# Kernel tuning notes

Hardware: AMD Instinct MI355X
Metric: run time of the kernel (lower is better)

Reference implementation:

```python
import jax, jax.numpy as jnp
import numpy as np

B, Q, H = 1, 1024, 2048
NH, NKV, HD = 32, 8, 64
KB = 2048
THETA = 10000.0
KB_MAX_TRAIN = 4096.0


def _bitlinear(x, w):
    """BitNet b1.58 linear: per-token int8 absmax activation quant + ternary weight quant (STE)."""
    a_scale = 127.0 / jnp.clip(jnp.max(jnp.abs(x), axis=-1, keepdims=True), 1e-5)
    xq = jnp.clip(jnp.round(x * a_scale), -128.0, 127.0) / a_scale
    w_scale = 1.0 / jnp.clip(jnp.mean(jnp.abs(w)), 1e-5)
    wq = jnp.clip(jnp.round(w * w_scale), -1.0, 1.0) / w_scale
    x_ste = x + jax.lax.stop_gradient(xq - x)
    w_ste = w + jax.lax.stop_gradient(wq - w)
    return jnp.einsum('bsh,oh->bso', x_ste, w_ste)


def _rope_cos_sin(position_ids):
    inv_freq = 1.0 / (THETA ** (jnp.arange(0, HD, 2, dtype=jnp.float32) / HD))  # [HD/2]
    freqs = position_ids.astype(jnp.float32)[..., None] * inv_freq  # [B,Q,HD/2]
    emb = jnp.concatenate([freqs, freqs], axis=-1)  # [B,Q,HD]
    return jnp.cos(emb)[:, None], jnp.sin(emb)[:, None]  # [B,1,Q,HD]


def _rotate_half(x):
    return jnp.concatenate([-x[..., HD // 2:], x[..., :HD // 2]], axis=-1)


def setup_inputs() -> dict:
    key = jax.random.key(0)
    ks = jax.random.split(key, 9)
    hidden_states = jax.random.normal(ks[0], (B, Q, H), jnp.float32)
    # additive causal mask
    attention_mask = jnp.triu(jnp.full((Q, Q), -1e9, jnp.float32), 1)[None, None]
    kb_keys = jax.random.normal(ks[1], (B, NH, KB, HD), jnp.float32)
    kb_values = jax.random.normal(ks[2], (B, NH, KB, HD), jnp.float32)
    s = 0.02
    Wq = jax.random.normal(ks[3], (NH * HD, H), jnp.float32) * s
    Wk = jax.random.normal(ks[4], (NKV * HD, H), jnp.float32) * s
    Wv = jax.random.normal(ks[5], (NKV * HD, H), jnp.float32) * s
    Wo = jax.random.normal(ks[6], (H, NH * HD), jnp.float32) * s
    Wq_new = jax.random.normal(ks[7], (NH * HD, H), jnp.float32) * s
    position_ids = jnp.arange(Q, dtype=jnp.int32)[None, :]
    return dict(hidden_states=hidden_states, attention_mask=attention_mask,
                kb_keys=kb_keys, kb_values=kb_values,
                Wq=Wq, Wk=Wk, Wv=Wv, Wo=Wo, Wq_new=Wq_new,
                position_ids=position_ids)


def reference(hidden_states, attention_mask, kb_keys, kb_values,
              Wq, Wk, Wv, Wo, Wq_new, position_ids):
    b, q_len, _ = hidden_states.shape
    # BitLinear QKV projections
    q = _bitlinear(hidden_states, Wq).reshape(b, q_len, NH, HD).transpose(0, 2, 1, 3)
    k = _bitlinear(hidden_states, Wk).reshape(b, q_len, NKV, HD).transpose(0, 2, 1, 3)
    v = _bitlinear(hidden_states, Wv).reshape(b, q_len, NKV, HD).transpose(0, 2, 1, 3)
    # RoPE on prompt q/k (KB query is NOT rotated, matching the source)
    cos, sin = _rope_cos_sin(position_ids)
    q = q * cos + _rotate_half(q) * sin
    k = k * cos + _rotate_half(k) * sin
    # GQA: repeat kv heads
    groups = NH // NKV
    k = jnp.repeat(k, groups, axis=1)
    v = jnp.repeat(v, groups, axis=1)
    # KB query via separate BitLinear
    kb_q = _bitlinear(hidden_states, Wq_new).reshape(b, q_len, NH, HD).transpose(0, 2, 1, 3)
    scale = 1.0 / jnp.sqrt(jnp.float32(HD))
    kb_len = kb_keys.shape[2]
    scores_kb = jnp.einsum('bhqd,bhkd->bhqk', kb_q, kb_keys) * scale
    scores_kb = scores_kb + (jnp.log(jnp.float32(KB_MAX_TRAIN)) - jnp.log(jnp.float32(kb_len)))
    scores_p = jnp.einsum('bhqd,bhkd->bhqk', q, k) * scale + attention_mask
    attn = jax.nn.softmax(jnp.concatenate([scores_kb, scores_p], axis=-1).astype(jnp.float32), axis=-1)
    out = (jnp.einsum('bhqk,bhkd->bhqd', attn[..., :kb_len], kb_values)
           + jnp.einsum('bhqk,bhkd->bhqd', attn[..., kb_len:], v))
    out = out.transpose(0, 2, 1, 3).reshape(b, q_len, NH * HD)
    return _bitlinear(out, Wo)
```

## Files before the change

kernel.cpp:

```cpp
#include <hip/hip_runtime.h>
#include <hip/hip_bf16.h>
#include <stdint.h>
#include <math.h>

#define cH    2048
#define cQ    1024
#define cNH   32
#define cNKV  8
#define cKB   2048

#define INV_BIG   (1.0f/4194304.0f)
#define INV_SMALL (1.0f/1048576.0f)

#define WS_SUMS 0
#define WS_DQ1  256
#define WS_DQ2  4352
#define WS_XQ   8448
#define WS_WALL 4202752
#define WS_QB   25174272
#define WS_KB   33562880
#define WS_VB   35660032
#define WS_QN   37757184
#define WS_ROPET 46145792

using short8  = __attribute__((ext_vector_type(8))) short;
using floatx4 = __attribute__((ext_vector_type(4))) float;

__device__ __forceinline__ void bsplit(float x, unsigned short& hi, unsigned short& lo) {
  __hip_bfloat16 h = __float2bfloat16(x);
  float hf = __bfloat162float(h);
  __hip_bfloat16 l = __float2bfloat16(x - hf);
  hi = *(unsigned short*)&h;
  lo = *(unsigned short*)&l;
}

__device__ __forceinline__ unsigned short tern(float v, float ws) {
  float q = rintf(v * ws);
  q = fminf(fmaxf(q, -1.0f), 1.0f);
  return (unsigned short)(__float_as_uint(q) >> 16);
}

__device__ __forceinline__ void gload16(const void* g, void* l) {
  __builtin_amdgcn_global_load_lds((const __attribute__((address_space(1))) void*)g,
                                   (__attribute__((address_space(3))) void*)l, 16, 0, 0);
}

__global__ void k_ropetab(const int* __restrict__ pos, float2* __restrict__ tab) {
  int i = blockIdx.x * 256 + threadIdx.x;
  int t = i >> 5, d = i & 31;
  double p = (double)pos[t];
  double ang = p * pow(10000.0, -(double)d / 32.0);
  tab[i] = make_float2((float)cos(ang), (float)sin(ang));
}

__global__ void k_abssum5(const float* __restrict__ w0, const float* __restrict__ w1,
                          const float* __restrict__ w2, const float* __restrict__ w3,
                          const float* __restrict__ w4, double* __restrict__ out) {
  __shared__ double red[256];
  const int seg = blockIdx.y;
  const float* w = seg == 0 ? w0 : seg == 1 ? w1 : seg == 2 ? w2 : seg == 3 ? w3 : w4;
  const int n4 = ((seg == 1 || seg == 2) ? 512 * 2048 : 2048 * 2048) / 4;
  double s = 0.0;
  for (int i = blockIdx.x * 256 + threadIdx.x; i < n4; i += gridDim.x * 256) {
    float4 x = *(const float4*)(w + (size_t)i * 4);
    s += (double)fabsf(x.x) + (double)fabsf(x.y) + (double)fabsf(x.z) + (double)fabsf(x.w);
  }
  red[threadIdx.x] = s;
  __syncthreads();
  for (int o = 128; o > 0; o >>= 1) {
    if ((int)threadIdx.x < o) red[threadIdx.x] += red[threadIdx.x + o];
    __syncthreads();
  }
  if (threadIdx.x == 0) atomicAdd(out + seg, red[0]);
}

__global__ void k_wquant4(const float* __restrict__ Wq, const float* __restrict__ Wk,
                          const float* __restrict__ Wv, const float* __restrict__ Wqn,
                          unsigned short* __restrict__ wall, const double* __restrict__ sums) {
  size_t i = ((size_t)blockIdx.x * 256 + threadIdx.x) * 4;
  const float* src; size_t off; double s; float inv;
  if (i < 4194304)      { src = Wq;  off = 0;       s = sums[0]; inv = INV_BIG; }
  else if (i < 5242880) { src = Wk;  off = 4194304; s = sums[1]; inv = INV_SMALL; }
  else if (i < 6291456) { src = Wv;  off = 5242880; s = sums[2]; inv = INV_SMALL; }
  else                  { src = Wqn; off = 6291456; s = sums[4]; inv = INV_BIG; }
  float ws = 1.0f / fmaxf((float)s * inv, 1e-5f);
  float4 x = *(const float4*)(src + (i - off));
  ushort4 o;
  o.x = tern(x.x, ws); o.y = tern(x.y, ws); o.z = tern(x.z, ws); o.w = tern(x.w, ws);
  *(ushort4*)(wall + i) = o;
}

__global__ void k_wquant(const float* __restrict__ w, unsigned short* __restrict__ wq,
                         const double* __restrict__ sum, float inv_n) {
  size_t i = ((size_t)blockIdx.x * 256 + threadIdx.x) * 4;
  float ws = 1.0f / fmaxf((float)(*sum) * inv_n, 1e-5f);
  float4 x = *(const float4*)(w + i);
  ushort4 o;
  o.x = tern(x.x, ws); o.y = tern(x.y, ws); o.z = tern(x.z, ws); o.w = tern(x.w, ws);
  *(ushort4*)(wq + i) = o;
}

__global__ void k_aquant(const float* __restrict__ x, unsigned short* __restrict__ xq,
                         float* __restrict__ dq, int K) {
  int t = blockIdx.x;
  const float4* xr = (const float4*)(x + (size_t)t * K);
  const int K4 = K / 4;
  __shared__ float red[256];
  float m = 0.0f;
  for (int i = threadIdx.x; i < K4; i += 256) {
    float4 v = xr[i];
    m = fmaxf(m, fmaxf(fmaxf(fabsf(v.x), fabsf(v.y)), fmaxf(fabsf(v.z), fabsf(v.w))));
  }
  red[threadIdx.x] = m;
  __syncthreads();
  for (int o = 128; o > 0; o >>= 1) {
    if ((int)threadIdx.x < o) red[threadIdx.x] = fmaxf(red[threadIdx.x], red[threadIdx.x + o]);
    __syncthreads();
  }
  float amax = fmaxf(red[0], 1e-5f);
  float as = 127.0f / amax;
  ushort4* xo = (ushort4*)(xq + (size_t)t * K);
  for (int i = threadIdx.x; i < K4; i += 256) {
    float4 v = xr[i];
    ushort4 o;
    float q;
    q = fminf(fmaxf(rintf(v.x * as), -128.0f), 127.0f); o.x = (unsigned short)(__float_as_uint(q) >> 16);
    q = fminf(fmaxf(rintf(v.y * as), -128.0f), 127.0f); o.y = (unsigned short)(__float_as_uint(q) >> 16);
    q = fminf(fmaxf(rintf(v.z * as), -128.0f), 127.0f); o.z = (unsigned short)(__float_as_uint(q) >> 16);
    q = fminf(fmaxf(rintf(v.w * as), -128.0f), 127.0f); o.w = (unsigned short)(__float_as_uint(q) >> 16);
    xo[i] = o;
  }
  if (threadIdx.x == 0) dq[t] = amax / 127.0f;
}

__global__ __launch_bounds__(256) void k_gemm_mfma(
    const unsigned short* __restrict__ Aq, const unsigned short* __restrict__ Ball,
    const float* __restrict__ adq, const double* __restrict__ sums,
    const float2* __restrict__ ropetab,
    float* __restrict__ oQ, unsigned short* __restrict__ oKhi,
    unsigned short* __restrict__ oKlo,
    float* __restrict__ oV, float* __restrict__ oQN, int mode) {
  __shared__ unsigned short As[128 * 72];
  __shared__ unsigned short Bs[128 * 72];
  const int t = threadIdx.x;
  const int lane = t & 63;
  const int row16 = lane & 15, q = lane >> 4;
  const int w = t >> 6;
  const int wm = (w >> 1) * 64, wn = (w & 1) * 64;
  const int bx = blockIdx.x;
  const int m0 = blockIdx.y * 128;
  const unsigned short* Bp = Ball + (size_t)bx * 128 * 2048;

  floatx4 acc[4][4];
#pragma unroll
  for (int g = 0; g < 4; ++g)
#pragma unroll
    for (int h = 0; h < 4; ++h) acc[g][h] = (floatx4){0.f, 0.f, 0.f, 0.f};

  for (int k0 = 0; k0 < 2048; k0 += 64) {
#pragma unroll
    for (int i = 0; i < 4; ++i) {
      int c = t + 256 * i;
      int row = c >> 3, g8 = c & 7;
      *(uint4*)&As[row * 72 + g8 * 8] =
          *(const uint4*)(Aq + (size_t)(m0 + row) * 2048 + k0 + g8 * 8);
      *(uint4*)&Bs[row * 72 + g8 * 8] =
          *(const uint4*)(Bp + (size_t)row * 2048 + k0 + g8 * 8);
    }
    __syncthreads();
#pragma unroll
    for (int kk = 0; kk < 2; ++kk) {
      short8 af[4], bf[4];
#pragma unroll
      for (int g = 0; g < 4; ++g)
        af[g] = *(const short8*)&As[(wm + g * 16 + row16) * 72 + kk * 32 + q * 8];
#pragma unroll
      for (int h = 0; h < 4; ++h)
        bf[h] = *(const short8*)&Bs[(wn + h * 16 + row16) * 72 + kk * 32 + q * 8];
#pragma unroll
      for (int g = 0; g < 4; ++g)
#pragma unroll
        for (int h = 0; h < 4; ++h)
          acc[g][h] = __builtin_amdgcn_mfma_f32_16x16x32_bf16(af[g], bf[h], acc[g][h], 0, 0, 0);
    }
    __syncthreads();
  }

  float* outp = nullptr; int Nout = 0, nb0; float wdq;
  if (mode == 1)      { outp = oQ;  Nout = 2048; nb0 = bx * 128;        wdq = fmaxf((float)sums[3] * INV_BIG,   1e-5f); }
  else if (bx < 16)   { outp = oQ;  Nout = 2048; nb0 = bx * 128;        wdq = fmaxf((float)sums[0] * INV_BIG,   1e-5f); }
  else if (bx < 20)   {             Nout = 512;  nb0 = (bx - 16) * 128; wdq = fmaxf((float)sums[1] * INV_SMALL, 1e-5f); }
  else if (bx < 24)   { outp = oV;  Nout = 512;  nb0 = (bx - 20) * 128; wdq = fmaxf((float)sums[2] * INV_SMALL, 1e-5f); }
  else                { outp = oQN; Nout = 2048; nb0 = (bx - 24) * 128; wdq = fmaxf((float)sums[4] * INV_BIG,   1e-5f); }

  if (mode == 0 && bx < 20) {
#pragma unroll
    for (int g = 0; g < 4; ++g)
#pragma unroll
      for (int r = 0; r < 4; ++r) {
        int m = m0 + wm + g * 16 + q * 4 + r;
        float s = adq[m] * wdq;
        float2 cs0 = ropetab[m * 32 + row16];
        float2 cs1 = ropetab[m * 32 + 16 + row16];
        float v0 = acc[g][0][r] * s, v1 = acc[g][1][r] * s;
        float v2 = acc[g][2][r] * s, v3 = acc[g][3][r] * s;
        float o0 = v0 * cs0.x - v2 * cs0.y;
        float o2 = v2 * cs0.x + v0 * cs0.y;
        float o1 = v1 * cs1.x - v3 * cs1.y;
        float o3 = v3 * cs1.x + v1 * cs1.y;
        if (bx < 16) {
          size_t base = (size_t)m * Nout + nb0 + wn;
          outp[base + row16]      = o0;
          outp[base + 16 + row16] = o1;
          outp[base + 32 + row16] = o2;
          outp[base + 48 + row16] = o3;
        } else {
          int hkv_ = (nb0 + wn) >> 6;
          int kt_ = m >> 6, rr = m & 63, sb = rr & 7;
          size_t tb = ((size_t)(hkv_ * 16 + kt_)) * 4096 + (size_t)rr * 64;
          int s0 = row16 >> 3, j0 = row16 & 7;
          unsigned short hi, lo; int ix;
          bsplit(o0, hi, lo); ix = (((0 + s0) ^ sb) << 3) + j0; oKhi[tb + ix] = hi; oKlo[tb + ix] = lo;
          bsplit(o1, hi, lo); ix = (((2 + s0) ^ sb) << 3) + j0; oKhi[tb + ix] = hi; oKlo[tb + ix] = lo;
          bsplit(o2, hi, lo); ix = (((4 + s0) ^ sb) << 3) + j0; oKhi[tb + ix] = hi; oKlo[tb + ix] = lo;
          bsplit(o3, hi, lo); ix = (((6 + s0) ^ sb) << 3) + j0; oKhi[tb + ix] = hi; oKlo[tb + ix] = lo;
        }
      }
  } else {
#pragma unroll
    for (int g = 0; g < 4; ++g)
#pragma unroll
      for (int r = 0; r < 4; ++r) {
        int m = m0 + wm + g * 16 + q * 4 + r;
        float s = adq[m] * wdq;
#pragma unroll
        for (int h = 0; h < 4; ++h)
          outp[(size_t)m * Nout + nb0 + wn + h * 16 + row16] = acc[g][h][r] * s;
      }
  }
}

__global__ __launch_bounds__(256) void k_prep(
    const float* __restrict__ kbv, const float* __restrict__ Vb,
    unsigned short* __restrict__ vtKBhi, unsigned short* __restrict__ vtPhi,
    float* __restrict__ kbk) {
  const int b = blockIdx.x;
  const int t = threadIdx.x;
  if (b >= 1152) {
    float* tile = kbk + (size_t)(b - 1152) * 4096;
    float v[2][8];
#pragma unroll
    for (int u = 0; u < 2; ++u) {
      int task = t + 256 * u;
      int r = task >> 3, s = task & 7;
      *(float4*)&v[u][0] = *(const float4*)(tile + r * 64 + s * 8);
      *(float4*)&v[u][4] = *(const float4*)(tile + r * 64 + s * 8 + 4);
    }
    __syncthreads();
    unsigned short* up = (unsigned short*)tile;
#pragma unroll
    for (int u = 0; u < 2; ++u) {
      int task = t + 256 * u;
      int r = task >> 3, s = task & 7;
      union { unsigned short u16[8]; uint4 q; } hi, lo;
#pragma unroll
      for (int j = 0; j < 8; ++j) bsplit(v[u][j], hi.u16[j], lo.u16[j]);
      size_t off = (size_t)r * 64 + ((s ^ (r & 7)) << 3);
      *(uint4*)(up + off)        = hi.q;
      *(uint4*)(up + 4096 + off) = lo.q;
    }
    return;
  }
  __shared__ float Lf[64 * 65];
  const float* src; unsigned short *dhi, *dlo; int srcStride;
  if (b < 1024) {
    int h = b >> 5, kt = b & 31;
    src = kbv + ((size_t)h * cKB + kt * 64) * 64; srcStride = 64;
    dhi = vtKBhi + (size_t)b * 4096; dlo = dhi + 4194304;
  } else {
    int bb = b - 1024;
    int hkv = bb >> 4, kt = bb & 15;
    src = Vb + (size_t)(kt * 64) * 512 + hkv * 64; srcStride = 512;
    dhi = vtPhi + (size_t)bb * 4096; dlo = dhi + 524288;
  }
#pragma unroll
  for (int i = 0; i < 4; ++i) {
    int c = t + 256 * i;
    int row = c >> 4, c4 = (c & 15) * 4;
    float4 x = *(const float4*)(src + (size_t)row * srcStride + c4);
    Lf[row * 65 + c4 + 0] = x.x;
    Lf[row * 65 + c4 + 1] = x.y;
    Lf[row * 65 + c4 + 2] = x.z;
    Lf[row * 65 + c4 + 3] = x.w;
  }
  __syncthreads();
#pragma unroll
  for (int u = 0; u < 2; ++u) {
    int task = t + 256 * u;
    int d = task >> 3, s = task & 7;
    union { unsigned short u16[8]; uint4 q; } hi, lo;
#pragma unroll
    for (int j = 0; j < 8; ++j) bsplit(Lf[(s * 8 + j) * 65 + d], hi.u16[j], lo.u16[j]);
    size_t off = (size_t)d * 64 + ((s ^ (d & 7)) << 3);
    *(uint4*)(dhi + off) = hi.q;
    *(uint4*)(dlo + off) = lo.q;
  }
}

__global__ __launch_bounds__(256, 3) void k_attn_mfma(
    const float* __restrict__ Qr, float* qnctx,
    const unsigned short* __restrict__ KPhi,
    const unsigned short* __restrict__ kbkS,
    const unsigned short* __restrict__ vtKBhi,
    const unsigned short* __restrict__ vtPhi) {
  __shared__ __attribute__((aligned(16))) unsigned short Khi[4096], Klo[4096];
  __shared__ __attribute__((aligned(16))) unsigned short Vhi[4096], Vlo[4096];
  __shared__ __attribute__((aligned(16))) unsigned int Pbuf[4][16 * 68];

  const int t = threadIdx.x;
  const int lane = t & 63;
  const int col = lane & 15;
  const int quad = lane >> 4;
  const int w = t >> 6;
  const int h = blockIdx.x;
  const int q0 = blockIdx.y * 64;
  const int hkv = h >> 2;
  const float kbbias = 0.69314718055994531f;
  unsigned int* Pw = &Pbuf[w][0];
  const int cb = col * 64;
  const int sw0 = ((quad    ) ^ (col & 7)) << 3;
  const int sw1 = ((quad + 4) ^ (col & 7)) << 3;
  const int so = w * 1024 + lane * 8;

  short8 qh[2], ql[2];
  auto load_q = [&](const float* base) {
#pragma unroll
    for (int kk = 0; kk < 2; ++kk) {
      const float* p = base + (size_t)(q0 + w * 16 + col) * 2048 + h * 64 + kk * 32 + quad * 8;
      float4 a = *(const float4*)p;
      float4 b = *(const float4*)(p + 4);
      float xs[8] = {a.x, a.y, a.z, a.w, b.x, b.y, b.z, b.w};
#pragma unroll
      for (int j = 0; j < 8; ++j) {
        unsigned short hi, lo;
        bsplit(xs[j] * 0.125f, hi, lo);
        qh[kk][j] = (short)hi;
        ql[kk][j] = (short)lo;
      }
    }
  };
  load_q(qnctx);

  floatx4 acco[4];
  float m_[4], l_[4];
#pragma unroll
  for (int nt = 0; nt < 4; ++nt) acco[nt] = (floatx4){0.f, 0.f, 0.f, 0.f};
#pragma unroll
  for (int r = 0; r < 4; ++r) { m_[r] = -3.0e38f; l_[r] = 0.f; }

  const int ntiles = 32 + (q0 >> 6) + 1;
  for (int kt = 0; kt < ntiles; ++kt) {
    const bool isKB = kt < 32;
    const int k0 = isKB ? kt * 64 : (kt - 32) * 64;
    if (kt == 32) load_q(Qr);

    {
      const unsigned short *sKhi, *sKlo, *sVhi, *sVlo;
      if (isKB) {
        const size_t tk = (size_t)(h * 32 + kt);
        sKhi = kbkS + tk * 8192;   sKlo = sKhi + 4096;
        sVhi = vtKBhi + tk * 4096; sVlo = sVhi + 4194304;
      } else {
        const size_t tk = (size_t)(hkv * 16 + (kt - 32));
        sKhi = KPhi + tk * 4096;   sKlo = sKhi + 524288;
        sVhi = vtPhi + tk * 4096;  sVlo = sVhi + 524288;
      }
      gload16(sKhi + so,       &Khi[w * 1024]);
      gload16(sKhi + so + 512, &Khi[w * 1024 + 512]);
      gload16(sKlo + so,       &Klo[w * 1024]);
      gload16(sKlo + so + 512, &Klo[w * 1024 + 512]);
      gload16(sVhi + so,       &Vhi[w * 1024]);
      gload16(sVhi + so + 512, &Vhi[w * 1024 + 512]);
      gload16(sVlo + so,       &Vlo[w * 1024]);
      gload16(sVlo + so + 512, &Vlo[w * 1024 + 512]);
    }
    __syncthreads();

    floatx4 accs[4];
#pragma unroll
    for (int nt = 0; nt < 4; ++nt) accs[nt] = (floatx4){0.f, 0.f, 0.f, 0.f};
#pragma unroll
    for (int kk = 0; kk < 2; ++kk) {
      const int swk = kk ? sw1 : sw0;
#pragma unroll
      for (int nt = 0; nt < 4; ++nt) {
        const int ko = nt * 1024 + cb + swk;
        short8 khh = *(const short8*)&Khi[ko];
        short8 kll = *(const short8*)&Klo[ko];
        accs[nt] = __builtin_amdgcn_mfma_f32_16x16x32_bf16(qh[kk], khh, accs[nt], 0, 0, 0);
        accs[nt] = __builtin_amdgcn_mfma_f32_16x16x32_bf16(ql[kk], khh, accs[nt], 0, 0, 0);
        accs[nt] = __builtin_amdgcn_mfma_f32_16x16x32_bf16(qh[kk], kll, accs[nt], 0, 0, 0);
      }
    }

    float sv[4][4];
#pragma unroll
    for (int nt = 0; nt < 4; ++nt) {
      int kg = k0 + nt * 16 + col;
#pragma unroll
      for (int r = 0; r < 4; ++r) {
        int qg = q0 + w * 16 + quad * 4 + r;
        float b = isKB ? kbbias : ((kg <= qg) ? 0.0f : -1e9f);
        sv[nt][r] = accs[nt][r] + b;
      }
    }
#pragma unroll
    for (int r = 0; r < 4; ++r) {
      float rmax = fmaxf(fmaxf(sv[0][r], sv[1][r]), fmaxf(sv[2][r], sv[3][r]));
#pragma unroll
      for (int off = 8; off; off >>= 1) rmax = fmaxf(rmax, __shfl_xor(rmax, off));
      float mnew = fmaxf(m_[r], rmax);
      float alpha = __expf(m_[r] - mnew);
      float psum = 0.f;
#pragma unroll
      for (int nt = 0; nt < 4; ++nt) {
        float p = __expf(sv[nt][r] - mnew);
        sv[nt][r] = p;
        psum += p;
      }
#pragma unroll
      for (int off = 8; off; off >>= 1) psum += __shfl_xor(psum, off);
      l_[r] = l_[r] * alpha + psum;
      m_[r] = mnew;
#pragma unroll
      for (int nt = 0; nt < 4; ++nt) acco[nt][r] *= alpha;
    }

#pragma unroll
    for (int nt = 0; nt < 4; ++nt)
#pragma unroll
      for (int r = 0; r < 4; ++r) {
        unsigned xb = __float_as_uint(sv[nt][r]);
        float hf = __uint_as_float(xb & 0xffff0000u);
        unsigned db = __float_as_uint(sv[nt][r] - hf);
        Pw[(quad * 4 + r) * 68 + nt * 16 + col] = (xb >> 16) | (db & 0xffff0000u);
      }

#pragma unroll
    for (int kk = 0; kk < 2; ++kk) {
      uint4 pa = *(const uint4*)&Pw[col * 68 + kk * 32 + quad * 8];
      uint4 pb = *(const uint4*)&Pw[col * 68 + kk * 32 + quad * 8 + 4];
      union { unsigned int u[4]; short8 s; } uh, ul;
      uh.u[0] = (pa.x & 0xffffu) | (pa.y << 16);
      uh.u[1] = (pa.z & 0xffffu) | (pa.w << 16);
      uh.u[2] = (pb.x & 0xffffu) | (pb.y << 16);
      uh.u[3] = (pb.z & 0xffffu) | (pb.w << 16);
      ul.u[0] = (pa.x >> 16) | (pa.y & 0xffff0000u);
      ul.u[1] = (pa.z >> 16) | (pa.w & 0xffff0000u);
      ul.u[2] = (pb.x >> 16) | (pb.y & 0xffff0000u);
      ul.u[3] = (pb.z >> 16) | (pb.w & 0xffff0000u);
      short8 ph8 = uh.s, pl8 = ul.s;
      const int swk = kk ? sw1 : sw0;
#pragma unroll
      for (int nt = 0; nt < 4; ++nt) {
        const int vo = nt * 1024 + cb + swk;
        short8 vhh = *(const short8*)&Vhi[vo];
        short8 vll = *(const short8*)&Vlo[vo];
        acco[nt] = __builtin_amdgcn_mfma_f32_16x16x32_bf16(ph8, vhh, acco[nt], 0, 0, 0);
        acco[nt] = __builtin_amdgcn_mfma_f32_16x16x32_bf16(pl8, vhh, acco[nt], 0, 0, 0);
        acco[nt] = __builtin_amdgcn_mfma_f32_16x16x32_bf16(ph8, vll, acco[nt], 0, 0, 0);
      }
    }
    __syncthreads();
  }

#pragma unroll
  for (int r = 0; r < 4; ++r) {
    float linv = 1.0f / l_[r];
#pragma unroll
    for (int nt = 0; nt < 4; ++nt)
      qnctx[(size_t)(q0 + w * 16 + quad * 4 + r) * 2048 + h * 64 + nt * 16 + col] =
          acco[nt][r] * linv;
  }
}

extern "C" void kernel_launch(void* const* d_in, const int* in_sizes, int n_in,
                              void* d_out, int out_size, void* d_ws, size_t ws_size,
                              hipStream_t stream) {
  (void)in_sizes; (void)n_in; (void)out_size; (void)ws_size;
  const float* hidden = (const float*)d_in[0];
  float* kbk = (float*)d_in[2];
  const float* kbv = (const float*)d_in[3];
  const float* Wq  = (const float*)d_in[4];
  const float* Wk  = (const float*)d_in[5];
  const float* Wv  = (const float*)d_in[6];
  const float* Wo  = (const float*)d_in[7];
  const float* Wqn = (const float*)d_in[8];
  const int*   pos = (const int*)d_in[9];

  char* ws = (char*)d_ws;
  double* sums = (double*)(ws + WS_SUMS);
  float* dq1 = (float*)(ws + WS_DQ1);
  float* dq2 = (float*)(ws + WS_DQ2);
  unsigned short* xq   = (unsigned short*)(ws + WS_XQ);
  unsigned short* wall = (unsigned short*)(ws + WS_WALL);
  unsigned short* vtKBhi = (unsigned short*)(ws + WS_WALL);
  unsigned short* vtPhi  = (unsigned short*)(ws + WS_WALL + 16777216);
  unsigned short* wqo  = (unsigned short*)(ws + WS_QB);
  float* Qb  = (float*)(ws + WS_QB);
  unsigned short* KPhi = (unsigned short*)(ws + WS_KB);
  unsigned short* KPlo = KPhi + 524288;
  float* Vb  = (float*)(ws + WS_VB);
  float* QNC = (float*)(ws + WS_QN);
  float2* ropetab = (float2*)(ws + WS_ROPET);

  hipMemsetAsync(sums, 0, 64, stream);

  k_ropetab<<<128, 256, 0, stream>>>(pos, ropetab);
  k_abssum5<<<dim3(128, 5), 256, 0, stream>>>(Wq, Wk, Wv, Wo, Wqn, sums);
  k_wquant4<<<10240, 256, 0, stream>>>(Wq, Wk, Wv, Wqn, wall, sums);
  k_aquant<<<cQ, 256, 0, stream>>>(hidden, xq, dq1, cH);

  k_gemm_mfma<<<dim3(40, 8), 256, 0, stream>>>(xq, wall, dq1, sums, ropetab,
                                               Qb, KPhi, KPlo, Vb, QNC, 0);

  k_prep<<<1152 + 1024, 256, 0, stream>>>(kbv, Vb, vtKBhi, vtPhi, kbk);

  k_attn_mfma<<<dim3(cNH, cQ / 64), 256, 0, stream>>>(
      Qb, QNC, KPhi, (const unsigned short*)kbk, vtKBhi, vtPhi);

  k_wquant<<<4096, 256, 0, stream>>>(Wo, wqo, sums + 3, INV_BIG);
  k_aquant<<<cQ, 256, 0, stream>>>(QNC, xq, dq2, cH);

  k_gemm_mfma<<<dim3(16, 8), 256, 0, stream>>>(xq, wqo, dq2, sums, ropetab,
                                               (float*)d_out, nullptr, nullptr,
                                               nullptr, nullptr, 1);
}
```

Baseline: 396.7 us.

## Double-buffer K/V tiles in attention kernel with async prefetch and priority hints

Doubles the LDS K/V buffers so the next tile's global-to-LDS loads are issued before computing on the current tile, replacing __syncthreads with explicit vmcnt waits and barriers. Both Q variants are loaded up front, mask arithmetic is specialized so only the diagonal tile applies causal masking, the P buffer uses an XOR swizzle instead of padding, and s_setprio wraps the MFMA blocks. The larger LDS footprint lowers launch bounds from 3 to 2 blocks per CU, trading occupancy for overlap. The extra Q registers add register pressure.

```diff
diff --git a/kernel.cpp b/kernel.cpp
--- a/kernel.cpp
+++ b/kernel.cpp
@@ -307,15 +307,15 @@
   }
 }
 
-__global__ __launch_bounds__(256, 3) void k_attn_mfma(
+__global__ __launch_bounds__(256, 2) void k_attn_mfma(
     const float* __restrict__ Qr, float* qnctx,
     const unsigned short* __restrict__ KPhi,
     const unsigned short* __restrict__ kbkS,
     const unsigned short* __restrict__ vtKBhi,
     const unsigned short* __restrict__ vtPhi) {
-  __shared__ __attribute__((aligned(16))) unsigned short Khi[4096], Klo[4096];
-  __shared__ __attribute__((aligned(16))) unsigned short Vhi[4096], Vlo[4096];
-  __shared__ __attribute__((aligned(16))) unsigned int Pbuf[4][16 * 68];
+  __shared__ __attribute__((aligned(16))) unsigned short Khi[2][4096], Klo[2][4096];
+  __shared__ __attribute__((aligned(16))) unsigned short Vhi[2][4096], Vlo[2][4096];
+  __shared__ __attribute__((aligned(16))) unsigned int Pbuf[4][16 * 64];
 
   const int t = threadIdx.x;
   const int lane = t & 63;
@@ -332,24 +332,59 @@
   const int sw1 = ((quad + 4) ^ (col & 7)) << 3;
   const int so = w * 1024 + lane * 8;
 
-  short8 qh[2], ql[2];
-  auto load_q = [&](const float* base) {
+  const int prow = quad * 4;
+  const int pf_r = col & 7;
+  const int prd0 = col * 64;
+
+  short8 qAh[2], qAl[2];
+  short8 qBh[2], qBl[2];
+  {
+    const float* baseA = qnctx;
+    const float* baseB = Qr;
 #pragma unroll
     for (int kk = 0; kk < 2; ++kk) {
-      const float* p = base + (size_t)(q0 + w * 16 + col) * 2048 + h * 64 + kk * 32 + quad * 8;
-      float4 a = *(const float4*)p;
-      float4 b = *(const float4*)(p + 4);
+      const size_t off = (size_t)(q0 + w * 16 + col) * 2048 + h * 64 + kk * 32 + quad * 8;
+      float4 a = *(const float4*)(baseA + off);
+      float4 b = *(const float4*)(baseA + off + 4);
       float xs[8] = {a.x, a.y, a.z, a.w, b.x, b.y, b.z, b.w};
 #pragma unroll
       for (int j = 0; j < 8; ++j) {
         unsigned short hi, lo;
         bsplit(xs[j] * 0.125f, hi, lo);
-        qh[kk][j] = (short)hi;
-        ql[kk][j] = (short)lo;
-      }
-    }
+        qAh[kk][j] = (short)hi; qAl[kk][j] = (short)lo;
+      }
+      float4 c = *(const float4*)(baseB + off);
+      float4 d = *(const float4*)(baseB + off + 4);
+      float ys[8] = {c.x, c.y, c.z, c.w, d.x, d.y, d.z, d.w};
+#pragma unroll
+      for (int j = 0; j < 8; ++j) {
+        unsigned short hi, lo;
+        bsplit(ys[j] * 0.125f, hi, lo);
+        qBh[kk][j] = (short)hi; qBl[kk][j] = (short)lo;
+      }
+    }
+  }
+
+  auto stage = [&](int kt2, int bsel) {
+    const unsigned short *sKhi, *sKlo, *sVhi, *sVlo;
+    if (kt2 < 32) {
+      const size_t tk = (size_t)(h * 32 + kt2);
+      sKhi = kbkS + tk * 8192;   sKlo = sKhi + 4096;
+      sVhi = vtKBhi + tk * 4096; sVlo = sVhi + 4194304;
+    } else {
+      const size_t tk = (size_t)(hkv * 16 + (kt2 - 32));
+      sKhi = KPhi + tk * 4096;   sKlo = sKhi + 524288;
+      sVhi = vtPhi + tk * 4096;  sVlo = sVhi + 524288;
+    }
+    gload16(sKhi + so,       &Khi[bsel][w * 1024]);
+    gload16(sKhi + so + 512, &Khi[bsel][w * 1024 + 512]);
+    gload16(sKlo + so,       &Klo[bsel][w * 1024]);
+    gload16(sKlo + so + 512, &Klo[bsel][w * 1024 + 512]);
+    gload16(sVhi + so,       &Vhi[bsel][w * 1024]);
+    gload16(sVhi + so + 512, &Vhi[bsel][w * 1024 + 512]);
+    gload16(sVlo + so,       &Vlo[bsel][w * 1024]);
+    gload16(sVlo + so + 512, &Vlo[bsel][w * 1024 + 512]);
   };
-  load_q(qnctx);
 
   floatx4 acco[4];
   float m_[4], l_[4];
@@ -359,59 +394,73 @@
   for (int r = 0; r < 4; ++r) { m_[r] = -3.0e38f; l_[r] = 0.f; }
 
   const int ntiles = 32 + (q0 >> 6) + 1;
+  stage(0, 0);
+
   for (int kt = 0; kt < ntiles; ++kt) {
+    const int cur = kt & 1;
     const bool isKB = kt < 32;
     const int k0 = isKB ? kt * 64 : (kt - 32) * 64;
-    if (kt == 32) load_q(Qr);
-
-    {
-      const unsigned short *sKhi, *sKlo, *sVhi, *sVlo;
-      if (isKB) {
-        const size_t tk = (size_t)(h * 32 + kt);
-        sKhi = kbkS + tk * 8192;   sKlo = sKhi + 4096;
-        sVhi = vtKBhi + tk * 4096; sVlo = sVhi + 4194304;
-      } else {
-        const size_t tk = (size_t)(hkv * 16 + (kt - 32));
-        sKhi = KPhi + tk * 4096;   sKlo = sKhi + 524288;
-        sVhi = vtPhi + tk * 4096;  sVlo = sVhi + 524288;
-      }
-      gload16(sKhi + so,       &Khi[w * 1024]);
-      gload16(sKhi + so + 512, &Khi[w * 1024 + 512]);
-      gload16(sKlo + so,       &Klo[w * 1024]);
-      gload16(sKlo + so + 512, &Klo[w * 1024 + 512]);
-      gload16(sVhi + so,       &Vhi[w * 1024]);
-      gload16(sVhi + so + 512, &Vhi[w * 1024 + 512]);
-      gload16(sVlo + so,       &Vlo[w * 1024]);
-      gload16(sVlo + so + 512, &Vlo[w * 1024 + 512]);
-    }
-    __syncthreads();
+    const int pfkt = (kt + 1 < ntiles) ? kt + 1 : kt;
+    stage(pfkt, cur ^ 1);
+    asm volatile("s_waitcnt vmcnt(8)" ::: "memory");
+    __builtin_amdgcn_s_barrier();
+    asm volatile("" ::: "memory");
 
     floatx4 accs[4];
 #pragma unroll
     for (int nt = 0; nt < 4; ++nt) accs[nt] = (floatx4){0.f, 0.f, 0.f, 0.f};
-#pragma unroll
-    for (int kk = 0; kk < 2; ++kk) {
-      const int swk = kk ? sw1 : sw0;
+    __builtin_amdgcn_s_setprio(1);
+    if (isKB) {
+#pragma unroll
+      for (int kk = 0; kk < 2; ++kk) {
+        const int swk = kk ? sw1 : sw0;
+#pragma unroll
+        for (int nt = 0; nt < 4; ++nt) {
+          const int ko = nt * 1024 + cb + swk;
+          short8 khh = *(const short8*)&Khi[cur][ko];
+          short8 kll = *(const short8*)&Klo[cur][ko];
+          accs[nt] = __builtin_amdgcn_mfma_f32_16x16x32_bf16(qAh[kk], khh, accs[nt], 0, 0, 0);
+          accs[nt] = __builtin_amdgcn_mfma_f32_16x16x32_bf16(qAl[kk], khh, accs[nt], 0, 0, 0);
+          accs[nt] = __builtin_amdgcn_mfma_f32_16x16x32_bf16(qAh[kk], kll, accs[nt], 0, 0, 0);
+        }
+      }
+    } else {
+#pragma unroll
+      for (int kk = 0; kk < 2; ++kk) {
+        const int swk = kk ? sw1 : sw0;
+#pragma unroll
+        for (int nt = 0; nt < 4; ++nt) {
+          const int ko = nt * 1024 + cb + swk;
+          short8 khh = *(const short8*)&Khi[cur][ko];
+          short8 kll = *(const short8*)&Klo[cur][ko];
+          accs[nt] = __builtin_amdgcn_mfma_f32_16x16x32_bf16(qBh[kk], khh, accs[nt], 0, 0, 0);
+          accs[nt] = __builtin_amdgcn_mfma_f32_16x16x32_bf16(qBl[kk], khh, accs[nt], 0, 0, 0);
+          accs[nt] = __builtin_amdgcn_mfma_f32_16x16x32_bf16(qBh[kk], kll, accs[nt], 0, 0, 0);
+        }
+      }
+    }
+    __builtin_amdgcn_s_setprio(0);
+
+    float sv[4][4];
+    if (isKB) {
+#pragma unroll
+      for (int nt = 0; nt < 4; ++nt)
+#pragma unroll
+        for (int r = 0; r < 4; ++r) sv[nt][r] = accs[nt][r] + kbbias;
+    } else if (kt < ntiles - 1) {
+#pragma unroll
+      for (int nt = 0; nt < 4; ++nt)
+#pragma unroll
+        for (int r = 0; r < 4; ++r) sv[nt][r] = accs[nt][r];
+    } else {
 #pragma unroll
       for (int nt = 0; nt < 4; ++nt) {
-        const int ko = nt * 1024 + cb + swk;
-        short8 khh = *(const short8*)&Khi[ko];
-        short8 kll = *(const short8*)&Klo[ko];
-        accs[nt] = __builtin_amdgcn_mfma_f32_16x16x32_bf16(qh[kk], khh, accs[nt], 0, 0, 0);
-        accs[nt] = __builtin_amdgcn_mfma_f32_16x16x32_bf16(ql[kk], khh, accs[nt], 0, 0, 0);
-        accs[nt] = __builtin_amdgcn_mfma_f32_16x16x32_bf16(qh[kk], kll, accs[nt], 0, 0, 0);
-      }
-    }
-
-    float sv[4][4];
-#pragma unroll
-    for (int nt = 0; nt < 4; ++nt) {
-      int kg = k0 + nt * 16 + col;
-#pragma unroll
-      for (int r = 0; r < 4; ++r) {
-        int qg = q0 + w * 16 + quad * 4 + r;
-        float b = isKB ? kbbias : ((kg <= qg) ? 0.0f : -1e9f);
-        sv[nt][r] = accs[nt][r] + b;
+        int kl = nt * 16 + col;
+#pragma unroll
+        for (int r = 0; r < 4; ++r) {
+          int ql = w * 16 + quad * 4 + r;
+          sv[nt][r] = accs[nt][r] + ((kl <= ql) ? 0.0f : -1e9f);
+        }
       }
     }
 #pragma unroll
@@ -443,13 +492,17 @@
         unsigned xb = __float_as_uint(sv[nt][r]);
         float hf = __uint_as_float(xb & 0xffff0000u);
         unsigned db = __float_as_uint(sv[nt][r] - hf);
-        Pw[(quad * 4 + r) * 68 + nt * 16 + col] = (xb >> 16) | (db & 0xffff0000u);
+        int row = prow + r;
+        int cu = nt * 16 + col;
+        int slot = cu >> 2, j = cu & 3;
+        Pw[row * 64 + ((((slot ^ (row & 7)) << 2)) | j)] = (xb >> 16) | (db & 0xffff0000u);
       }
 
 #pragma unroll
     for (int kk = 0; kk < 2; ++kk) {
-      uint4 pa = *(const uint4*)&Pw[col * 68 + kk * 32 + quad * 8];
-      uint4 pb = *(const uint4*)&Pw[col * 68 + kk * 32 + quad * 8 + 4];
+      const int s0 = kk * 8 + quad * 2;
+      uint4 pa = *(const uint4*)&Pw[prd0 + (((s0) ^ pf_r) << 2)];
+      uint4 pb = *(const uint4*)&Pw[prd0 + (((s0 + 1) ^ pf_r) << 2)];
       union { unsigned int u[4]; short8 s; } uh, ul;
       uh.u[0] = (pa.x & 0xffffu) | (pa.y << 16);
       uh.u[1] = (pa.z & 0xffffu) | (pa.w << 16);
@@ -461,18 +514,23 @@
       ul.u[3] = (pb.z >> 16) | (pb.w & 0xffff0000u);
       short8 ph8 = uh.s, pl8 = ul.s;
       const int swk = kk ? sw1 : sw0;
+      __builtin_amdgcn_s_setprio(1);
 #pragma unroll
       for (int nt = 0; nt < 4; ++nt) {
         const int vo = nt * 1024 + cb + swk;
-        short8 vhh = *(const short8*)&Vhi[vo];
-        short8 vll = *(const short8*)&Vlo[vo];
+        short8 vhh = *(const short8*)&Vhi[cur][vo];
+        short8 vll = *(const short8*)&Vlo[cur][vo];
         acco[nt] = __builtin_amdgcn_mfma_f32_16x16x32_bf16(ph8, vhh, acco[nt], 0, 0, 0);
         acco[nt] = __builtin_amdgcn_mfma_f32_16x16x32_bf16(pl8, vhh, acco[nt], 0, 0, 0);
         acco[nt] = __builtin_amdgcn_mfma_f32_16x16x32_bf16(ph8, vll, acco[nt], 0, 0, 0);
       }
-    }
-    __syncthreads();
-  }
+      __builtin_amdgcn_s_setprio(0);
+    }
+    asm volatile("s_waitcnt lgkmcnt(0)" ::: "memory");
+    __builtin_amdgcn_s_barrier();
+    asm volatile("" ::: "memory");
+  }
+  asm volatile("s_waitcnt vmcnt(0)" ::: "memory");
 
 #pragma unroll
   for (int r = 0; r < 4; ++r) {
```

After: 405.3 us. 2.2% more time.

## Load K/V fragments directly into registers in MFMA-fragment layout, prefetch next K

Applied to the files above, without the earlier changes.

The prep and projection kernels now write K and V^T tiles in a layout that matches the per-lane MFMA operand order. The attention kernel then loads K/V fragments straight from global memory into registers instead of staging them through LDS. This removes the LDS staging buffers and most block barriers. The next K tile is prefetched during the softmax/PV phase, both query variants are kept in registers, and the causal mask is applied only on the diagonal tile. The cost is higher register pressure, so launch bounds drop occupancy from 3 to 2 blocks per CU, and each wave issues its own global loads with no LDS sharing.

```diff
diff --git a/kernel.cpp b/kernel.cpp
--- a/kernel.cpp
+++ b/kernel.cpp
@@ -23,6 +23,7 @@
 #define WS_QN   37757184
 #define WS_ROPET 46145792
 
+
 using short8  = __attribute__((ext_vector_type(8))) short;
 using floatx4 = __attribute__((ext_vector_type(4))) float;
 
@@ -38,11 +39,6 @@
   float q = rintf(v * ws);
   q = fminf(fmaxf(q, -1.0f), 1.0f);
   return (unsigned short)(__float_as_uint(q) >> 16);
-}
-
-__device__ __forceinline__ void gload16(const void* g, void* l) {
-  __builtin_amdgcn_global_load_lds((const __attribute__((address_space(1))) void*)g,
-                                   (__attribute__((address_space(3))) void*)l, 16, 0, 0);
 }
 
 __global__ void k_ropetab(const int* __restrict__ pos, float2* __restrict__ tab) {
@@ -216,14 +212,15 @@
           outp[base + 48 + row16] = o3;
         } else {
           int hkv_ = (nb0 + wn) >> 6;
-          int kt_ = m >> 6, rr = m & 63, sb = rr & 7;
-          size_t tb = ((size_t)(hkv_ * 16 + kt_)) * 4096 + (size_t)rr * 64;
-          int s0 = row16 >> 3, j0 = row16 & 7;
+          int kt_ = m >> 6, rr = m & 63;
+          size_t tb = ((size_t)(hkv_ * 16 + kt_)) * 4096;
+          int lbase = (rr & 15) + ((row16 >> 3) << 4);
+          int ntb = (rr >> 4) * 512 + (row16 & 7);
           unsigned short hi, lo; int ix;
-          bsplit(o0, hi, lo); ix = (((0 + s0) ^ sb) << 3) + j0; oKhi[tb + ix] = hi; oKlo[tb + ix] = lo;
-          bsplit(o1, hi, lo); ix = (((2 + s0) ^ sb) << 3) + j0; oKhi[tb + ix] = hi; oKlo[tb + ix] = lo;
-          bsplit(o2, hi, lo); ix = (((4 + s0) ^ sb) << 3) + j0; oKhi[tb + ix] = hi; oKlo[tb + ix] = lo;
-          bsplit(o3, hi, lo); ix = (((6 + s0) ^ sb) << 3) + j0; oKhi[tb + ix] = hi; oKlo[tb + ix] = lo;
+          bsplit(o0, hi, lo); ix = ntb + (lbase     ) * 8;          oKhi[tb + ix] = hi; oKlo[tb + ix] = lo;
+          bsplit(o1, hi, lo); ix = ntb + (lbase + 32) * 8;          oKhi[tb + ix] = hi; oKlo[tb + ix] = lo;
+          bsplit(o2, hi, lo); ix = ntb + (lbase     ) * 8 + 2048;   oKhi[tb + ix] = hi; oKlo[tb + ix] = lo;
+          bsplit(o3, hi, lo); ix = ntb + (lbase + 32) * 8 + 2048;   oKhi[tb + ix] = hi; oKlo[tb + ix] = lo;
         }
       }
   } else {
@@ -265,7 +262,7 @@
       union { unsigned short u16[8]; uint4 q; } hi, lo;
 #pragma unroll
       for (int j = 0; j < 8; ++j) bsplit(v[u][j], hi.u16[j], lo.u16[j]);
-      size_t off = (size_t)r * 64 + ((s ^ (r & 7)) << 3);
+      size_t off = (size_t)(((s >> 2) * 4 + (r >> 4)) * 512 + ((r & 15) + ((s & 3) << 4)) * 8);
       *(uint4*)(up + off)        = hi.q;
       *(uint4*)(up + 4096 + off) = lo.q;
     }
@@ -301,20 +298,18 @@
     union { unsigned short u16[8]; uint4 q; } hi, lo;
 #pragma unroll
     for (int j = 0; j < 8; ++j) bsplit(Lf[(s * 8 + j) * 65 + d], hi.u16[j], lo.u16[j]);
-    size_t off = (size_t)d * 64 + ((s ^ (d & 7)) << 3);
+    size_t off = (size_t)(((s >> 2) * 4 + (d >> 4)) * 512 + ((d & 15) + ((s & 3) << 4)) * 8);
     *(uint4*)(dhi + off) = hi.q;
     *(uint4*)(dlo + off) = lo.q;
   }
 }
 
-__global__ __launch_bounds__(256, 3) void k_attn_mfma(
+__global__ __launch_bounds__(256, 2) void k_attn_mfma(
     const float* __restrict__ Qr, float* qnctx,
     const unsigned short* __restrict__ KPhi,
     const unsigned short* __restrict__ kbkS,
     const unsigned short* __restrict__ vtKBhi,
     const unsigned short* __restrict__ vtPhi) {
-  __shared__ __attribute__((aligned(16))) unsigned short Khi[4096], Klo[4096];
-  __shared__ __attribute__((aligned(16))) unsigned short Vhi[4096], Vlo[4096];
   __shared__ __attribute__((aligned(16))) unsigned int Pbuf[4][16 * 68];
 
   const int t = threadIdx.x;
@@ -327,29 +322,34 @@
   const int hkv = h >> 2;
   const float kbbias = 0.69314718055994531f;
   unsigned int* Pw = &Pbuf[w][0];
-  const int cb = col * 64;
-  const int sw0 = ((quad    ) ^ (col & 7)) << 3;
-  const int sw1 = ((quad + 4) ^ (col & 7)) << 3;
-  const int so = w * 1024 + lane * 8;
-
-  short8 qh[2], ql[2];
-  auto load_q = [&](const float* base) {
+  const int fl = lane * 8;
+
+  short8 qAh[2], qAl[2];
+  short8 qBh[2], qBl[2];
+  {
 #pragma unroll
     for (int kk = 0; kk < 2; ++kk) {
-      const float* p = base + (size_t)(q0 + w * 16 + col) * 2048 + h * 64 + kk * 32 + quad * 8;
-      float4 a = *(const float4*)p;
-      float4 b = *(const float4*)(p + 4);
+      const size_t off = (size_t)(q0 + w * 16 + col) * 2048 + h * 64 + kk * 32 + quad * 8;
+      float4 a = *(const float4*)(qnctx + off);
+      float4 b = *(const float4*)(qnctx + off + 4);
       float xs[8] = {a.x, a.y, a.z, a.w, b.x, b.y, b.z, b.w};
 #pragma unroll
       for (int j = 0; j < 8; ++j) {
         unsigned short hi, lo;
         bsplit(xs[j] * 0.125f, hi, lo);
-        qh[kk][j] = (short)hi;
-        ql[kk][j] = (short)lo;
-      }
-    }
-  };
-  load_q(qnctx);
+        qAh[kk][j] = (short)hi; qAl[kk][j] = (short)lo;
+      }
+      float4 c = *(const float4*)(Qr + off);
+      float4 d = *(const float4*)(Qr + off + 4);
+      float ys[8] = {c.x, c.y, c.z, c.w, d.x, d.y, d.z, d.w};
+#pragma unroll
+      for (int j = 0; j < 8; ++j) {
+        unsigned short hi, lo;
+        bsplit(ys[j] * 0.125f, hi, lo);
+        qBh[kk][j] = (short)hi; qBl[kk][j] = (short)lo;
+      }
+    }
+  }
 
   floatx4 acco[4];
   float m_[4], l_[4];
@@ -359,59 +359,89 @@
   for (int r = 0; r < 4; ++r) { m_[r] = -3.0e38f; l_[r] = 0.f; }
 
   const int ntiles = 32 + (q0 >> 6) + 1;
+
+  short8 kh[2][4], kl[2][4];
+  short8 vh[2][4], vl[2][4];
+
+  auto loadK = [&](int kt2) {
+    const unsigned short *ph, *pl;
+    if (kt2 < 32) { const size_t tk = (size_t)(h * 32 + kt2);
+                    ph = kbkS + tk * 8192; pl = ph + 4096; }
+    else          { const size_t tk = (size_t)(hkv * 16 + (kt2 - 32));
+                    ph = KPhi + tk * 4096; pl = ph + 524288; }
+#pragma unroll
+    for (int kk = 0; kk < 2; ++kk)
+#pragma unroll
+      for (int nt = 0; nt < 4; ++nt) {
+        kh[kk][nt] = *(const short8*)(ph + (kk * 4 + nt) * 512 + fl);
+        kl[kk][nt] = *(const short8*)(pl + (kk * 4 + nt) * 512 + fl);
+      }
+  };
+  auto loadV = [&](int kt2) {
+    const unsigned short *ph, *pl;
+    if (kt2 < 32) { const size_t tk = (size_t)(h * 32 + kt2);
+                    ph = vtKBhi + tk * 4096; pl = ph + 4194304; }
+    else          { const size_t tk = (size_t)(hkv * 16 + (kt2 - 32));
+                    ph = vtPhi + tk * 4096; pl = ph + 524288; }
+#pragma unroll
+    for (int kk = 0; kk < 2; ++kk)
+#pragma unroll
+      for (int nt = 0; nt < 4; ++nt) {
+        vh[kk][nt] = *(const short8*)(ph + (kk * 4 + nt) * 512 + fl);
+        vl[kk][nt] = *(const short8*)(pl + (kk * 4 + nt) * 512 + fl);
+      }
+  };
+
+  loadK(0);
+
   for (int kt = 0; kt < ntiles; ++kt) {
     const bool isKB = kt < 32;
-    const int k0 = isKB ? kt * 64 : (kt - 32) * 64;
-    if (kt == 32) load_q(Qr);
-
-    {
-      const unsigned short *sKhi, *sKlo, *sVhi, *sVlo;
-      if (isKB) {
-        const size_t tk = (size_t)(h * 32 + kt);
-        sKhi = kbkS + tk * 8192;   sKlo = sKhi + 4096;
-        sVhi = vtKBhi + tk * 4096; sVlo = sVhi + 4194304;
-      } else {
-        const size_t tk = (size_t)(hkv * 16 + (kt - 32));
-        sKhi = KPhi + tk * 4096;   sKlo = sKhi + 524288;
-        sVhi = vtPhi + tk * 4096;  sVlo = sVhi + 524288;
-      }
-      gload16(sKhi + so,       &Khi[w * 1024]);
-      gload16(sKhi + so + 512, &Khi[w * 1024 + 512]);
-      gload16(sKlo + so,       &Klo[w * 1024]);
-      gload16(sKlo + so + 512, &Klo[w * 1024 + 512]);
-      gload16(sVhi + so,       &Vhi[w * 1024]);
-      gload16(sVhi + so + 512, &Vhi[w * 1024 + 512]);
-      gload16(sVlo + so,       &Vlo[w * 1024]);
-      gload16(sVlo + so + 512, &Vlo[w * 1024 + 512]);
-    }
-    __syncthreads();
+    loadV(kt);
+    __builtin_amdgcn_s_barrier();
 
     floatx4 accs[4];
 #pragma unroll
     for (int nt = 0; nt < 4; ++nt) accs[nt] = (floatx4){0.f, 0.f, 0.f, 0.f};
-#pragma unroll
-    for (int kk = 0; kk < 2; ++kk) {
-      const int swk = kk ? sw1 : sw0;
+    if (isKB) {
+#pragma unroll
+      for (int kk = 0; kk < 2; ++kk)
+#pragma unroll
+        for (int nt = 0; nt < 4; ++nt) {
+          accs[nt] = __builtin_amdgcn_mfma_f32_16x16x32_bf16(qAh[kk], kh[kk][nt], accs[nt], 0, 0, 0);
+          accs[nt] = __builtin_amdgcn_mfma_f32_16x16x32_bf16(qAl[kk], kh[kk][nt], accs[nt], 0, 0, 0);
+          accs[nt] = __builtin_amdgcn_mfma_f32_16x16x32_bf16(qAh[kk], kl[kk][nt], accs[nt], 0, 0, 0);
+        }
+    } else {
+#pragma unroll
+      for (int kk = 0; kk < 2; ++kk)
+#pragma unroll
+        for (int nt = 0; nt < 4; ++nt) {
+          accs[nt] = __builtin_amdgcn_mfma_f32_16x16x32_bf16(qBh[kk], kh[kk][nt], accs[nt], 0, 0, 0);
+          accs[nt] = __builtin_amdgcn_mfma_f32_16x16x32_bf16(qBl[kk], kh[kk][nt], accs[nt], 0, 0, 0);
+          accs[nt] = __builtin_amdgcn_mfma_f32_16x16x32_bf16(qBh[kk], kl[kk][nt], accs[nt], 0, 0, 0);
+        }
+    }
+
+    float sv[4][4];
+    if (isKB) {
+#pragma unroll
+      for (int nt = 0; nt < 4; ++nt)
+#pragma unroll
+        for (int r = 0; r < 4; ++r) sv[nt][r] = accs[nt][r] + kbbias;
+    } else if (kt < ntiles - 1) {
+#pragma unroll
+      for (int nt = 0; nt < 4; ++nt)
+#pragma unroll
+        for (int r = 0; r < 4; ++r) sv[nt][r] = accs[nt][r];
+    } else {
 #pragma unroll
       for (int nt = 0; nt < 4; ++nt) {
-        const int ko = nt * 1024 + cb + swk;
-        short8 khh = *(const short8*)&Khi[ko];
-        short8 kll = *(const short8*)&Klo[ko];
-        accs[nt] = __builtin_amdgcn_mfma_f32_16x16x32_bf16(qh[kk], khh, accs[nt], 0, 0, 0);
-        accs[nt] = __builtin_amdgcn_mfma_f32_16x16x32_bf16(ql[kk], khh, accs[nt], 0, 0, 0);
-        accs[nt] = __builtin_amdgcn_mfma_f32_16x16x32_bf16(qh[kk], kll, accs[nt], 0, 0, 0);
-      }
-    }
-
-    float sv[4][4];
-#pragma unroll
-    for (int nt = 0; nt < 4; ++nt) {
-      int kg = k0 + nt * 16 + col;
-#pragma unroll
-      for (int r = 0; r < 4; ++r) {
-        int qg = q0 + w * 16 + quad * 4 + r;
-        float b = isKB ? kbbias : ((kg <= qg) ? 0.0f : -1e9f);
-        sv[nt][r] = accs[nt][r] + b;
+        int kl_ = nt * 16 + col;
+#pragma unroll
+        for (int r = 0; r < 4; ++r) {
+          int ql_ = w * 16 + quad * 4 + r;
+          sv[nt][r] = accs[nt][r] + ((kl_ <= ql_) ? 0.0f : -1e9f);
+        }
       }
     }
 #pragma unroll
@@ -435,6 +465,8 @@
 #pragma unroll
       for (int nt = 0; nt < 4; ++nt) acco[nt][r] *= alpha;
     }
+
+    loadK(kt + 1 < ntiles ? kt + 1 : kt);
 
 #pragma unroll
     for (int nt = 0; nt < 4; ++nt)
@@ -460,18 +492,13 @@
       ul.u[2] = (pb.x >> 16) | (pb.y & 0xffff0000u);
       ul.u[3] = (pb.z >> 16) | (pb.w & 0xffff0000u);
       short8 ph8 = uh.s, pl8 = ul.s;
-      const int swk = kk ? sw1 : sw0;
 #pragma unroll
       for (int nt = 0; nt < 4; ++nt) {
-        const int vo = nt * 1024 + cb + swk;
-        short8 vhh = *(const short8*)&Vhi[vo];
-        short8 vll = *(const short8*)&Vlo[vo];
-        acco[nt] = __builtin_amdgcn_mfma_f32_16x16x32_bf16(ph8, vhh, acco[nt], 0, 0, 0);
-        acco[nt] = __builtin_amdgcn_mfma_f32_16x16x32_bf16(pl8, vhh, acco[nt], 0, 0, 0);
-        acco[nt] = __builtin_amdgcn_mfma_f32_16x16x32_bf16(ph8, vll, acco[nt], 0, 0, 0);
-      }
-    }
-    __syncthreads();
+        acco[nt] = __builtin_amdgcn_mfma_f32_16x16x32_bf16(ph8, vh[kk][nt], acco[nt], 0, 0, 0);
+        acco[nt] = __builtin_amdgcn_mfma_f32_16x16x32_bf16(pl8, vh[kk][nt], acco[nt], 0, 0, 0);
+        acco[nt] = __builtin_amdgcn_mfma_f32_16x16x32_bf16(ph8, vl[kk][nt], acco[nt], 0, 0, 0);
+      }
+    }
   }
 
 #pragma unroll
```

New measurement: 392.0 us. Within noise of the previous version (-1.2%).
